# Optimization experiments

Hardware: AMD Instinct MI355X
Metric: run time of the kernel (lower is better)

Reference implementation:

```python
import jax, jax.numpy as jnp
import numpy as np

B, F, T = 2, 512, 512
D, N, H = 1024, 16, 64   # hidden, heads, head_dim
K = 32                   # time-bias MLP kernal_size
FILT = 4096              # FFN filter size
L = 4                    # num_decoder_blocks
EPS = 1e-6


def _glorot(key, shape, fan_in, fan_out):
    lim = np.sqrt(6.0 / (fan_in + fan_out)).astype(np.float32)
    return jax.random.uniform(key, shape, jnp.float32, -lim, lim)


def setup_inputs() -> dict:
    key = jax.random.key(0)
    ks = jax.random.split(key, 18)
    inp = {
        'decoder_inputs': jax.random.normal(ks[0], (B, F, D), jnp.float32),
        'encoder_outputs': jax.random.normal(ks[1], (B, T, D), jnp.float32),
        'decoder_times_dist': jax.random.uniform(ks[2], (B, F, F), jnp.float32),
        'decoder_encoder_times_dist': jax.random.uniform(ks[3], (B, F, T), jnp.float32),
        'dec_self_attn_bias': jnp.zeros((B, 1, 1, F), jnp.float32),
        'enc_dec_attn_bias': jnp.zeros((B, 1, 1, T), jnp.float32),
        # per-block stacked parameters (leading dim L)
        'Wq': _glorot(ks[4], (L, D, N, H), D, D),
        'Wk': _glorot(ks[5], (L, D, N, H), D, D),
        'Wv': _glorot(ks[6], (L, D, N, H), D, D),
        'Wo': _glorot(ks[7], (L, N, H, D), D, D),
        'Wth': _glorot(ks[8], (L, 1, K), 1, K),
        'bth': jnp.zeros((L, K), jnp.float32),
        'Wto': _glorot(ks[9], (L, K, 1), K, 1),
        'bto': jnp.zeros((L, 1), jnp.float32),
        'Wf1': _glorot(ks[10], (L, D, FILT), D, FILT),
        'bf1': jnp.zeros((L, FILT), jnp.float32),
        'Wf2': _glorot(ks[11], (L, FILT, D), FILT, D),
        'bf2': jnp.zeros((L, D), jnp.float32),
    }
    return inp


def _norm(x):
    # non-trainable LayerNormalization: (x - mean) / (std + eps)
    m = jnp.mean(x, axis=-1, keepdims=True)
    s = jnp.sqrt(jnp.mean((x - m) ** 2, axis=-1, keepdims=True))
    return (x - m) / (s + EPS)


def _attention(x, src, dist, bias, Wq, Wk, Wv, Wo, Wth, bth, Wto, bto):
    q = jnp.einsum('bfd,dnh->bfnh', x, Wq) * (H ** -0.5)
    k = jnp.einsum('btd,dnh->btnh', src, Wk)
    v = jnp.einsum('btd,dnh->btnh', src, Wv)
    # learned time bias: [B,F,T,1] -> relu MLP(K) -> 1 -> [B,F,T]
    hbias = jax.nn.relu(dist[..., None] @ Wth + bth)        # [B,F,T,K]
    qs_bias = (hbias @ Wto + bto)[..., 0]                   # [B,F,T]
    logits = jnp.einsum('btnh,bfnh->bnft', k, q)            # [B,N,F,T]
    logits = logits + bias + qs_bias[:, None]
    w = jax.nn.softmax(logits, axis=-1)
    out = jnp.einsum('bnft,btnh->bfnh', w, v)
    return jnp.einsum('bfnh,nhd->bfd', out, Wo)


def reference(decoder_inputs, encoder_outputs, decoder_times_dist,
              decoder_encoder_times_dist, dec_self_attn_bias, enc_dec_attn_bias,
              Wq, Wk, Wv, Wo, Wth, bth, Wto, bto, Wf1, bf1, Wf2, bf2):
    # decoder_times_dist / dec_self_attn_bias are accepted but unused (as in source call)
    x = decoder_inputs
    for i in range(L):
        # enc-dec attention with pre-norm + residual
        y = _attention(_norm(x), encoder_outputs, decoder_encoder_times_dist,
                       enc_dec_attn_bias, Wq[i], Wk[i], Wv[i], Wo[i],
                       Wth[i], bth[i], Wto[i], bto[i])
        x = x + y
        # FFN with pre-norm + residual
        y = jax.nn.relu(_norm(x) @ Wf1[i] + bf1[i]) @ Wf2[i] + bf2[i]
        x = x + y
    return _norm(x)
```

## Files before the change

### kernel.cpp

```cpp
#include <hip/hip_runtime.h>

typedef unsigned short u16;
typedef __attribute__((ext_vector_type(8))) unsigned short u16x8;
typedef __attribute__((ext_vector_type(4))) unsigned short u16x4;
typedef __attribute__((ext_vector_type(4))) float f32x4;

#define DEVI __device__ __forceinline__

DEVI u16 f2bf(float f){
  unsigned u = __float_as_uint(f);
  u += 0x7FFFu + ((u >> 16) & 1u);
  return (u16)(u >> 16);
}

DEVI void gload16(const void* g, void* l){
  __builtin_amdgcn_global_load_lds((const __attribute__((address_space(1))) void*)g,
                                   (__attribute__((address_space(3))) void*)l, 16, 0, 0);
}

DEVI float wave_sum(float v){
#pragma unroll
  for (int o = 32; o; o >>= 1) v += __shfl_xor(v, o, 64);
  return v;
}

#define MFMA16(a,b,c) __builtin_amdgcn_mfma_f32_16x16x32_bf16((a),(b),(c),0,0,0)

__global__ __launch_bounds__(256) void f32_to_bf16_k(const float* __restrict__ in,
                                                     u16* __restrict__ out, int n4){
  int i = blockIdx.x * 256 + threadIdx.x;
  if (i < n4){
    float4 v = ((const float4*)in)[i];
    u16x4 o = { f2bf(v.x), f2bf(v.y), f2bf(v.z), f2bf(v.w) };
    ((u16x4*)out)[i] = o;
  }
}

__global__ __launch_bounds__(256) void trans_f32_bf16_k(const float* __restrict__ in0,
                                                        u16* __restrict__ out0, int R, int C){
  __shared__ u16 tile[32][33];
  const float* in = in0 + (size_t)blockIdx.z * R * C;
  u16* out = out0 + (size_t)blockIdx.z * R * C;
  const int c0 = blockIdx.x * 32, r0 = blockIdx.y * 32;
  const int tx = threadIdx.x & 31, ty = threadIdx.x >> 5;
#pragma unroll
  for (int k = 0; k < 4; k++)
    tile[ty + k*8][tx] = f2bf(in[(size_t)(r0 + ty + k*8) * C + c0 + tx]);
  __syncthreads();
#pragma unroll
  for (int k = 0; k < 4; k++)
    out[(size_t)(c0 + ty + k*8) * R + r0 + tx] = tile[tx][ty + k*8];
}

__global__ __launch_bounds__(256) void vtrans_k(const u16* __restrict__ V0, u16* __restrict__ Vt0){
  __shared__ u16 tile[32][33];
  const int t0 = blockIdx.x * 32;
  const int h0 = blockIdx.y * 32;
  const int z = blockIdx.z, l = z >> 5, bn = z & 31;
  const int b = bn >> 4, n = bn & 15;
  const u16* V = V0 + (size_t)l * 1048576;
  u16* Vt = Vt0 + (size_t)l * 1048576;
  const int tx = threadIdx.x & 31, ty = threadIdx.x >> 5;
#pragma unroll
  for (int k = 0; k < 4; k++)
    tile[ty + k*8][tx] = V[(size_t)(b*512 + t0 + ty + k*8) * 1024 + n*64 + h0 + tx];
  __syncthreads();
#pragma unroll
  for (int k = 0; k < 4; k++)
    Vt[(size_t)((b*16 + n)*64 + h0 + ty + k*8) * 512 + t0 + tx] = tile[tx][ty + k*8];
}

__global__ __launch_bounds__(256) void layernorm_k(const float* __restrict__ in, u16* __restrict__ outp){
  const int row = blockIdx.x;
  const int tid = threadIdx.x;
  const float4 v = ((const float4*)(in + (size_t)row * 1024))[tid];
  __shared__ float sb[8];
  const int wid = tid >> 6, lane = tid & 63;
  float s = wave_sum(v.x + v.y + v.z + v.w);
  if (lane == 0) sb[wid] = s;
  __syncthreads();
  const float mean = (sb[0] + sb[1] + sb[2] + sb[3]) * (1.0f / 1024.0f);
  const float dx = v.x - mean, dy = v.y - mean, dz = v.z - mean, dw = v.w - mean;
  float q = wave_sum(dx*dx + dy*dy + dz*dz + dw*dw);
  if (lane == 0) sb[4 + wid] = q;
  __syncthreads();
  const float sd = sqrtf((sb[4] + sb[5] + sb[6] + sb[7]) * (1.0f / 1024.0f));
  const float inv = 1.0f / (sd + 1e-6f);
  u16x4 o = { f2bf(dx*inv), f2bf(dy*inv), f2bf(dz*inv), f2bf(dw*inv) };
  ((u16x4*)outp)[(size_t)row * 256 + tid] = o;
}

__global__ __launch_bounds__(256) void qsbias_k(const float* __restrict__ dist,
    const float* __restrict__ Wth0, const float* __restrict__ bth0,
    const float* __restrict__ Wto0, const float* __restrict__ bto0,
    float* __restrict__ qs0){
  const int ly = blockIdx.y;
  const float* Wth = Wth0 + ly*32;
  const float* bth = bth0 + ly*32;
  const float* Wto = Wto0 + ly*32;
  float* qs = qs0 + (size_t)ly * 524288;
  const int idx = blockIdx.x * 256 + threadIdx.x;
  float4 s4 = ((const float4*)dist)[idx];
  float sv[4] = { s4.x, s4.y, s4.z, s4.w };
  float r[4];
  const float b0 = bto0[ly];
#pragma unroll
  for (int c = 0; c < 4; c++) r[c] = b0;
#pragma unroll
  for (int k = 0; k < 32; k++){
    const float wk = Wth[k], bk = bth[k], ok = Wto[k];
#pragma unroll
    for (int c = 0; c < 4; c++){
      float h = fmaxf(sv[c] * wk + bk, 0.0f);
      r[c] += h * ok;
    }
  }
  ((float4*)qs)[idx] = make_float4(r[0], r[1], r[2], r[3]);
}

template<int MODE>
DEVI void gemm128_core(const u16* A, int lda, const u16* Bt, int ldb,
                       int Klen, int Nd, void* Cout,
                       const float* bias, float scale,
                       u16* Als, u16* Bls, int row0, int col0){
  const int tid = threadIdx.x;
  const int wid = tid >> 6, lane = tid & 63;
  const int wm = wid >> 1, wn = wid & 1;
  const int lrow = lane & 15, g = lane >> 4, e7 = lane & 7;
  f32x4 acc[4][4] = {};

  const int scol = ((lane & 7) ^ ((lane >> 3) & 7)) * 8;
  const u16* Ag = A + (size_t)(row0 + wid*8 + (lane >> 3)) * lda + scol;
  const u16* Bg = Bt + (size_t)(col0 + wid*8 + (lane >> 3)) * ldb + scol;
  const int dst0 = wid * 512;

  const int nt = Klen >> 6;

#define STAGE128(buf, k0)                                                     \
  {                                                                           \
    _Pragma("unroll")                                                         \
    for (int q = 0; q < 4; q++){                                              \
      gload16(Ag + (size_t)q*32*lda + (k0), Als + (buf)*8192 + dst0 + q*2048);\
      gload16(Bg + (size_t)q*32*ldb + (k0), Bls + (buf)*8192 + dst0 + q*2048);\
    }                                                                         \
  }

  STAGE128(0, 0);
  __syncthreads();

  for (int t = 0; t < nt; t++){
    const int cur = t & 1;
    if (t + 1 < nt) STAGE128(cur ^ 1, (t + 1) << 6);
    const u16* Ab = Als + cur * 8192;
    const u16* Bb = Bls + cur * 8192;
#pragma unroll
    for (int ks = 0; ks < 2; ks++){
      const int sl = (((ks << 2) + g) ^ e7) << 3;
      u16x8 av[4], bv[4];
#pragma unroll
      for (int mi = 0; mi < 4; mi++)
        av[mi] = *(const u16x8*)(Ab + (wm*64 + mi*16 + lrow) * 64 + sl);
#pragma unroll
      for (int ni = 0; ni < 4; ni++)
        bv[ni] = *(const u16x8*)(Bb + (wn*64 + ni*16 + lrow) * 64 + sl);
#pragma unroll
      for (int mi = 0; mi < 4; mi++)
#pragma unroll
        for (int ni = 0; ni < 4; ni++)
          acc[mi][ni] = MFMA16(av[mi], bv[ni], acc[mi][ni]);
    }
    __syncthreads();
  }
#undef STAGE128

#pragma unroll
  for (int mi = 0; mi < 4; mi++){
#pragma unroll
    for (int ni = 0; ni < 4; ni++){
      const int col = col0 + wn*64 + ni*16 + lrow;
#pragma unroll
      for (int j = 0; j < 4; j++){
        const int row = row0 + wm*64 + mi*16 + g*4 + j;
        float v = acc[mi][ni][j];
        if (MODE == 3) v = fmaxf(v + bias[col], 0.0f);
        if (MODE == 0 || MODE == 3)
          ((u16*)Cout)[(size_t)row * Nd + col] = f2bf(v);
        else
          ((float*)Cout)[(size_t)row * Nd + col] = v;
      }
    }
  }
}

template<int MODE>
__global__ __launch_bounds__(256) void gemm128_k(const u16* __restrict__ A, int lda,
    const u16* __restrict__ Bt, int ldb, int Klen, int Nd, void* __restrict__ Cout,
    const float* __restrict__ bias, float scale){
  __shared__ __align__(16) u16 Als[2 * 8192];
  __shared__ __align__(16) u16 Bls[2 * 8192];
  gemm128_core<MODE>(A, lda, Bt, ldb, Klen, Nd, Cout, bias, scale,
                     Als, Bls, blockIdx.y * 128, blockIdx.x * 128);
}

__global__ __launch_bounds__(256) void gemmKV_k(const u16* __restrict__ encb,
    const u16* __restrict__ Wkt, const u16* __restrict__ Wvt,
    u16* __restrict__ Kb, u16* __restrict__ Vb){
  __shared__ __align__(16) u16 Als[2 * 8192];
  __shared__ __align__(16) u16 Bls[2 * 8192];
  const int z = blockIdx.z, l = z >> 1;
  const u16* Bt = ((z & 1) ? Wvt : Wkt) + (size_t)l * 1048576;
  u16* out = ((z & 1) ? Vb : Kb) + (size_t)l * 1048576;
  gemm128_core<0>(encb, 1024, Bt, 1024, 1024, 1024, out, nullptr, 1.0f,
                  Als, Bls, blockIdx.y * 128, blockIdx.x * 128);
}

__global__ __launch_bounds__(256) void gemm_splitk_k(const u16* __restrict__ A, int lda,
    const u16* __restrict__ Bt, int ldb, int Klen, float* __restrict__ part){
  __shared__ __align__(16) u16 Als[2 * 8192];
  __shared__ __align__(16) u16 Bls[2 * 8192];
  const int z = blockIdx.z;
  gemm128_core<5>(A + (size_t)z * Klen, lda, Bt + (size_t)z * Klen, ldb, Klen, 1024,
                  part + (size_t)z * 1048576, nullptr, 1.0f,
                  Als, Bls, blockIdx.y * 128, blockIdx.x * 128);
}

__global__ __launch_bounds__(256) void reduce4_bf16_k(const float* __restrict__ part,
                                                      u16* __restrict__ out, float scale){
  const int idx = blockIdx.x * 256 + threadIdx.x;
  float4 p0 = ((const float4*)part)[idx];
  float4 p1 = ((const float4*)(part + 1048576))[idx];
  float4 p2 = ((const float4*)(part + 2097152))[idx];
  float4 p3 = ((const float4*)(part + 3145728))[idx];
  u16x4 o = { f2bf((p0.x + p1.x + p2.x + p3.x) * scale),
              f2bf((p0.y + p1.y + p2.y + p3.y) * scale),
              f2bf((p0.z + p1.z + p2.z + p3.z) * scale),
              f2bf((p0.w + p1.w + p2.w + p3.w) * scale) };
  ((u16x4*)out)[idx] = o;
}

template<int BIAS, int LAST>
__global__ __launch_bounds__(256) void reduce_ln_k(const float* __restrict__ part,
    const float* __restrict__ bias, float* __restrict__ x, u16* __restrict__ xn,
    float* __restrict__ dout){
  const int row = blockIdx.x, tid = threadIdx.x;
  const size_t idx = (size_t)row * 256 + tid;
  float4 v = ((const float4*)x)[idx];
  float4 p0 = ((const float4*)part)[idx];
  float4 p1 = ((const float4*)(part + 1048576))[idx];
  float4 p2 = ((const float4*)(part + 2097152))[idx];
  float4 p3 = ((const float4*)(part + 3145728))[idx];
  v.x += p0.x + p1.x + p2.x + p3.x;
  v.y += p0.y + p1.y + p2.y + p3.y;
  v.z += p0.z + p1.z + p2.z + p3.z;
  v.w += p0.w + p1.w + p2.w + p3.w;
  if (BIAS){
    const float4 b = *(const float4*)(bias + tid * 4);
    v.x += b.x; v.y += b.y; v.z += b.z; v.w += b.w;
  }
  if (!LAST) ((float4*)x)[idx] = v;

  __shared__ float sb[8];
  const int wid = tid >> 6, lane = tid & 63;
  float s = wave_sum(v.x + v.y + v.z + v.w);
  if (lane == 0) sb[wid] = s;
  __syncthreads();
  const float mean = (sb[0] + sb[1] + sb[2] + sb[3]) * (1.0f / 1024.0f);
  const float dx = v.x - mean, dy = v.y - mean, dz = v.z - mean, dw = v.w - mean;
  float q = wave_sum(dx*dx + dy*dy + dz*dz + dw*dw);
  if (lane == 0) sb[4 + wid] = q;
  __syncthreads();
  const float sd = sqrtf((sb[4] + sb[5] + sb[6] + sb[7]) * (1.0f / 1024.0f));
  const float inv = 1.0f / (sd + 1e-6f);
  if (LAST){
    ((float4*)dout)[idx] = make_float4(dx*inv, dy*inv, dz*inv, dw*inv);
  } else {
    u16x4 o = { f2bf(dx*inv), f2bf(dy*inv), f2bf(dz*inv), f2bf(dw*inv) };
    ((u16x4*)xn)[idx] = o;
  }
}

__global__ __launch_bounds__(256, 1) void attn_k(const u16* __restrict__ Q,
    const u16* __restrict__ Kb, const u16* __restrict__ Vt,
    const float* __restrict__ qs, const float* __restrict__ abias,
    u16* __restrict__ aout){
  const int n = blockIdx.x, f0 = blockIdx.y * 64, b = blockIdx.z;
  const int w = threadIdx.x >> 6, lane = threadIdx.x & 63;
  const int l15 = lane & 15, g = lane >> 4, e7 = lane & 7;
  const int fw = f0 + w * 16;
  __shared__ __align__(16) u16 Pl[4][16 * 512];
  u16* pw = &Pl[w][0];

  const u16* qp = Q + ((size_t)b*512 + fw + l15) * 1024 + n*64 + g*8;
  const u16x8 qf0 = *(const u16x8*)qp;
  const u16x8 qf1 = *(const u16x8*)(qp + 32);

  f32x4 acc[32];
  const u16* kp = Kb + ((size_t)b*512 + l15) * 1024 + n*64 + g*8;
#pragma unroll
  for (int tf = 0; tf < 32; tf++){
    u16x8 k0 = *(const u16x8*)(kp + (size_t)tf*16*1024);
    u16x8 k1 = *(const u16x8*)(kp + (size_t)tf*16*1024 + 32);
    f32x4 z = {0.f, 0.f, 0.f, 0.f};
    z = MFMA16(k0, qf0, z);
    acc[tf] = MFMA16(k1, qf1, z);
  }

  const float* qsp = qs + ((size_t)b*512 + fw + l15) * 512 + g*4;
  const float* abp = abias + (size_t)b*512 + g*4;
  float m = -3.0e38f;
#pragma unroll
  for (int tf = 0; tf < 32; tf++){
    float4 qv = *(const float4*)(qsp + tf*16);
    float4 av = *(const float4*)(abp + tf*16);
    acc[tf][0] += qv.x + av.x;
    acc[tf][1] += qv.y + av.y;
    acc[tf][2] += qv.z + av.z;
    acc[tf][3] += qv.w + av.w;
    m = fmaxf(m, fmaxf(fmaxf(acc[tf][0], acc[tf][1]), fmaxf(acc[tf][2], acc[tf][3])));
  }
  m = fmaxf(m, __shfl_xor(m, 16, 64));
  m = fmaxf(m, __shfl_xor(m, 32, 64));

  float s = 0.f;
#pragma unroll
  for (int tf = 0; tf < 32; tf++){
#pragma unroll
    for (int j = 0; j < 4; j++){
      float e = __expf(acc[tf][j] - m);
      acc[tf][j] = e; s += e;
    }
  }
  s += __shfl_xor(s, 16, 64);
  s += __shfl_xor(s, 32, 64);
  const float inv = 1.0f / s;
  float invj[4];
#pragma unroll
  for (int j = 0; j < 4; j++) invj[j] = __shfl(inv, g*4 + j, 64);

#pragma unroll
  for (int tf = 0; tf < 32; tf++){
    const int chunk = tf*2 + (g >> 1);
    const int boff = (l15 << 10) + ((chunk ^ e7) << 4) + ((g & 1) << 3);
    u16x4 pk = { f2bf(acc[tf][0]), f2bf(acc[tf][1]), f2bf(acc[tf][2]), f2bf(acc[tf][3]) };
    *(u16x4*)((char*)pw + boff) = pk;
  }

  f32x4 oacc[4] = {};
  const u16* vp = Vt + ((size_t)(b*16 + n)*64 + l15) * 512 + g*8;
  for (int kk = 0; kk < 16; kk++){
    u16x8 pa = *(const u16x8*)((char*)pw + (l15 << 10) + ((((kk << 2) + g) ^ e7) << 4));
#pragma unroll
    for (int nf = 0; nf < 4; nf++){
      u16x8 vb = *(const u16x8*)(vp + (size_t)nf*16*512 + kk*32);
      oacc[nf] = MFMA16(pa, vb, oacc[nf]);
    }
  }

  u16* op = aout + ((size_t)b*512 + fw + g*4) * 1024 + n*64 + l15;
#pragma unroll
  for (int nf = 0; nf < 4; nf++)
#pragma unroll
    for (int j = 0; j < 4; j++)
      op[(size_t)j*1024 + nf*16] = f2bf(oacc[nf][j] * invj[j]);
}

extern "C" void kernel_launch(void* const* d_in, const int* in_sizes, int n_in,
                              void* d_out, int out_size, void* d_ws, size_t ws_size,
                              hipStream_t stream){
  const float* dec_in   = (const float*)d_in[0];
  const float* enc      = (const float*)d_in[1];
  const float* dist     = (const float*)d_in[3];
  const float* abias    = (const float*)d_in[5];
  const float* Wq  = (const float*)d_in[6];
  const float* Wk  = (const float*)d_in[7];
  const float* Wv  = (const float*)d_in[8];
  const float* Wo  = (const float*)d_in[9];
  const float* Wth = (const float*)d_in[10];
  const float* bth = (const float*)d_in[11];
  const float* Wto = (const float*)d_in[12];
  const float* bto = (const float*)d_in[13];
  const float* Wf1 = (const float*)d_in[14];
  const float* bf1 = (const float*)d_in[15];
  const float* Wf2 = (const float*)d_in[16];
  const float* bf2 = (const float*)d_in[17];
  float* dout = (float*)d_out;

  char* wp = (char*)d_ws;
  auto alloc = [&](size_t n) -> char* {
    char* p = wp; wp += (n + 255) & ~(size_t)255; return p;
  };
  float* x     = (float*)alloc((size_t)1048576 * 4);
  u16*  xn     = (u16*)alloc((size_t)1048576 * 2);
  u16*  encb   = (u16*)alloc((size_t)1048576 * 2);
  u16*  Wqt    = (u16*)alloc((size_t)4194304 * 2);
  u16*  Wkt    = (u16*)alloc((size_t)4194304 * 2);
  u16*  Wvt    = (u16*)alloc((size_t)4194304 * 2);
  u16*  Wot    = (u16*)alloc((size_t)4194304 * 2);
  u16*  Wf1t   = (u16*)alloc((size_t)16777216 * 2);
  u16*  Wf2t   = (u16*)alloc((size_t)16777216 * 2);
  u16*  Kb     = (u16*)alloc((size_t)4194304 * 2);
  u16*  Vb     = (u16*)alloc((size_t)4194304 * 2);
  u16*  Vt     = (u16*)alloc((size_t)4194304 * 2);
  u16*  Qb     = (u16*)alloc((size_t)1048576 * 2);
  float* qs    = (float*)alloc((size_t)2097152 * 4);
  u16*  aout   = (u16*)alloc((size_t)1048576 * 2);
  u16*  ffh    = (u16*)alloc((size_t)4194304 * 2);
  float* part  = (float*)alloc((size_t)4194304 * 4);

  hipMemcpyAsync(x, dec_in, (size_t)1048576 * 4, hipMemcpyDeviceToDevice, stream);
  f32_to_bf16_k<<<1024, 256, 0, stream>>>(enc, encb, 262144);

  trans_f32_bf16_k<<<dim3(32, 32, 4), 256, 0, stream>>>(Wq, Wqt, 1024, 1024);
  trans_f32_bf16_k<<<dim3(32, 32, 4), 256, 0, stream>>>(Wk, Wkt, 1024, 1024);
  trans_f32_bf16_k<<<dim3(32, 32, 4), 256, 0, stream>>>(Wv, Wvt, 1024, 1024);
  trans_f32_bf16_k<<<dim3(32, 32, 4), 256, 0, stream>>>(Wo, Wot, 1024, 1024);
  trans_f32_bf16_k<<<dim3(128, 32, 4), 256, 0, stream>>>(Wf1, Wf1t, 1024, 4096);
  trans_f32_bf16_k<<<dim3(32, 128, 4), 256, 0, stream>>>(Wf2, Wf2t, 4096, 1024);

  qsbias_k<<<dim3(512, 4), 256, 0, stream>>>(dist, Wth, bth, Wto, bto, qs);

  gemmKV_k<<<dim3(8, 8, 8), 256, 0, stream>>>(encb, Wkt, Wvt, Kb, Vb);
  vtrans_k<<<dim3(16, 2, 128), 256, 0, stream>>>(Vb, Vt);

  layernorm_k<<<1024, 256, 0, stream>>>(x, xn);

  for (int i = 0; i < 4; i++){
    const size_t wo = (size_t)i * 1048576;

    gemm_splitk_k<<<dim3(8, 8, 4), 256, 0, stream>>>(xn, 1024, Wqt + wo, 1024, 256, part);
    reduce4_bf16_k<<<1024, 256, 0, stream>>>(part, Qb, 0.125f);

    attn_k<<<dim3(16, 8, 2), 256, 0, stream>>>(Qb, Kb + wo, Vt + wo,
                                               qs + (size_t)i * 524288, abias, aout);

    gemm_splitk_k<<<dim3(8, 8, 4), 256, 0, stream>>>(aout, 1024, Wot + wo, 1024, 256, part);
    reduce_ln_k<0, 0><<<1024, 256, 0, stream>>>(part, nullptr, x, xn, nullptr);

    gemm128_k<3><<<dim3(32, 8), 256, 0, stream>>>(xn, 1024, Wf1t + (size_t)i*4194304, 1024,
                                                  1024, 4096, ffh, bf1 + (size_t)i*4096, 1.0f);
    gemm_splitk_k<<<dim3(8, 8, 4), 256, 0, stream>>>(ffh, 4096, Wf2t + (size_t)i*4194304, 4096,
                                                     1024, part);
    if (i < 3)
      reduce_ln_k<1, 0><<<1024, 256, 0, stream>>>(part, bf2 + (size_t)i*1024, x, xn, nullptr);
    else
      reduce_ln_k<1, 1><<<1024, 256, 0, stream>>>(part, bf2 + (size_t)i*1024, x, nullptr, dout);
  }
}
```

Measured before the change: 535.9 us.

## Shrink GEMM N-tile to 64, fold Q split-K reduce into attention, batch weight transposes

All GEMMs now use a 128x64 tile instead of 128x128, which doubles the grid size and gives more blocks to fill the device's CUs on these small problems. The separate reduce kernel for the Q projection is removed, and attention sums the four fp32 split-K partials and applies the scale directly when it loads Q. The four attention-weight transposes become one launch. In exchange, each GEMM block reuses its loaded data less, and every attention block reads fp32 partials from global memory redundantly.

```diff
diff --git a/kernel.cpp b/kernel.cpp
--- a/kernel.cpp
+++ b/kernel.cpp
@@ -50,6 +50,26 @@
 #pragma unroll
   for (int k = 0; k < 4; k++)
     out[(size_t)(c0 + ty + k*8) * R + r0 + tx] = tile[tx][ty + k*8];
+}
+
+__global__ __launch_bounds__(256) void trans4_f32_bf16_k(
+    const float* __restrict__ Wq, const float* __restrict__ Wk,
+    const float* __restrict__ Wv, const float* __restrict__ Wo,
+    u16* __restrict__ Wqt, u16* __restrict__ Wkt,
+    u16* __restrict__ Wvt, u16* __restrict__ Wot){
+  __shared__ u16 tile[32][33];
+  const int z = blockIdx.z, sel = z >> 2, l = z & 3;
+  const float* in = (sel == 0 ? Wq : sel == 1 ? Wk : sel == 2 ? Wv : Wo) + (size_t)l * 1048576;
+  u16* out = (sel == 0 ? Wqt : sel == 1 ? Wkt : sel == 2 ? Wvt : Wot) + (size_t)l * 1048576;
+  const int c0 = blockIdx.x * 32, r0 = blockIdx.y * 32;
+  const int tx = threadIdx.x & 31, ty = threadIdx.x >> 5;
+#pragma unroll
+  for (int k = 0; k < 4; k++)
+    tile[ty + k*8][tx] = f2bf(in[(size_t)(r0 + ty + k*8) * 1024 + c0 + tx]);
+  __syncthreads();
+#pragma unroll
+  for (int k = 0; k < 4; k++)
+    out[(size_t)(c0 + ty + k*8) * 1024 + r0 + tx] = tile[tx][ty + k*8];
 }
 
 __global__ __launch_bounds__(256) void vtrans_k(const u16* __restrict__ V0, u16* __restrict__ Vt0){
@@ -118,16 +138,18 @@
   ((float4*)qs)[idx] = make_float4(r[0], r[1], r[2], r[3]);
 }
 
-template<int MODE>
+template<int MODE, int BN>
 DEVI void gemm128_core(const u16* A, int lda, const u16* Bt, int ldb,
                        int Klen, int Nd, void* Cout,
                        const float* bias, float scale,
                        u16* Als, u16* Bls, int row0, int col0){
+  constexpr int WN = BN / 2, FN = BN / 32;
+  constexpr int BSZ = BN * 64;
   const int tid = threadIdx.x;
   const int wid = tid >> 6, lane = tid & 63;
   const int wm = wid >> 1, wn = wid & 1;
   const int lrow = lane & 15, g = lane >> 4, e7 = lane & 7;
-  f32x4 acc[4][4] = {};
+  f32x4 acc[4][FN] = {};
 
   const int scol = ((lane & 7) ^ ((lane >> 3) & 7)) * 8;
   const u16* Ag = A + (size_t)(row0 + wid*8 + (lane >> 3)) * lda + scol;
@@ -139,10 +161,11 @@
 #define STAGE128(buf, k0)                                                     \
   {                                                                           \
     _Pragma("unroll")                                                         \
-    for (int q = 0; q < 4; q++){                                              \
+    for (int q = 0; q < 4; q++)                                               \
       gload16(Ag + (size_t)q*32*lda + (k0), Als + (buf)*8192 + dst0 + q*2048);\
-      gload16(Bg + (size_t)q*32*ldb + (k0), Bls + (buf)*8192 + dst0 + q*2048);\
-    }                                                                         \
+    _Pragma("unroll")                                                         \
+    for (int q = 0; q < BN/32; q++)                                           \
+      gload16(Bg + (size_t)q*32*ldb + (k0), Bls + (buf)*BSZ + dst0 + q*2048); \
   }
 
   STAGE128(0, 0);
@@ -152,21 +175,21 @@
     const int cur = t & 1;
     if (t + 1 < nt) STAGE128(cur ^ 1, (t + 1) << 6);
     const u16* Ab = Als + cur * 8192;
-    const u16* Bb = Bls + cur * 8192;
+    const u16* Bb = Bls + cur * BSZ;
 #pragma unroll
     for (int ks = 0; ks < 2; ks++){
       const int sl = (((ks << 2) + g) ^ e7) << 3;
-      u16x8 av[4], bv[4];
+      u16x8 av[4], bv[FN];
 #pragma unroll
       for (int mi = 0; mi < 4; mi++)
         av[mi] = *(const u16x8*)(Ab + (wm*64 + mi*16 + lrow) * 64 + sl);
 #pragma unroll
-      for (int ni = 0; ni < 4; ni++)
-        bv[ni] = *(const u16x8*)(Bb + (wn*64 + ni*16 + lrow) * 64 + sl);
+      for (int ni = 0; ni < FN; ni++)
+        bv[ni] = *(const u16x8*)(Bb + (wn*WN + ni*16 + lrow) * 64 + sl);
 #pragma unroll
       for (int mi = 0; mi < 4; mi++)
 #pragma unroll
-        for (int ni = 0; ni < 4; ni++)
+        for (int ni = 0; ni < FN; ni++)
           acc[mi][ni] = MFMA16(av[mi], bv[ni], acc[mi][ni]);
     }
     __syncthreads();
@@ -176,8 +199,8 @@
 #pragma unroll
   for (int mi = 0; mi < 4; mi++){
 #pragma unroll
-    for (int ni = 0; ni < 4; ni++){
-      const int col = col0 + wn*64 + ni*16 + lrow;
+    for (int ni = 0; ni < FN; ni++){
+      const int col = col0 + wn*WN + ni*16 + lrow;
 #pragma unroll
       for (int j = 0; j < 4; j++){
         const int row = row0 + wm*64 + mi*16 + g*4 + j;
@@ -197,45 +220,31 @@
     const u16* __restrict__ Bt, int ldb, int Klen, int Nd, void* __restrict__ Cout,
     const float* __restrict__ bias, float scale){
   __shared__ __align__(16) u16 Als[2 * 8192];
-  __shared__ __align__(16) u16 Bls[2 * 8192];
-  gemm128_core<MODE>(A, lda, Bt, ldb, Klen, Nd, Cout, bias, scale,
-                     Als, Bls, blockIdx.y * 128, blockIdx.x * 128);
+  __shared__ __align__(16) u16 Bls[2 * 4096];
+  gemm128_core<MODE, 64>(A, lda, Bt, ldb, Klen, Nd, Cout, bias, scale,
+                         Als, Bls, blockIdx.y * 128, blockIdx.x * 64);
 }
 
 __global__ __launch_bounds__(256) void gemmKV_k(const u16* __restrict__ encb,
     const u16* __restrict__ Wkt, const u16* __restrict__ Wvt,
     u16* __restrict__ Kb, u16* __restrict__ Vb){
   __shared__ __align__(16) u16 Als[2 * 8192];
-  __shared__ __align__(16) u16 Bls[2 * 8192];
+  __shared__ __align__(16) u16 Bls[2 * 4096];
   const int z = blockIdx.z, l = z >> 1;
   const u16* Bt = ((z & 1) ? Wvt : Wkt) + (size_t)l * 1048576;
   u16* out = ((z & 1) ? Vb : Kb) + (size_t)l * 1048576;
-  gemm128_core<0>(encb, 1024, Bt, 1024, 1024, 1024, out, nullptr, 1.0f,
-                  Als, Bls, blockIdx.y * 128, blockIdx.x * 128);
+  gemm128_core<0, 64>(encb, 1024, Bt, 1024, 1024, 1024, out, nullptr, 1.0f,
+                      Als, Bls, blockIdx.y * 128, blockIdx.x * 64);
 }
 
 __global__ __launch_bounds__(256) void gemm_splitk_k(const u16* __restrict__ A, int lda,
     const u16* __restrict__ Bt, int ldb, int Klen, float* __restrict__ part){
   __shared__ __align__(16) u16 Als[2 * 8192];
-  __shared__ __align__(16) u16 Bls[2 * 8192];
+  __shared__ __align__(16) u16 Bls[2 * 4096];
   const int z = blockIdx.z;
-  gemm128_core<5>(A + (size_t)z * Klen, lda, Bt + (size_t)z * Klen, ldb, Klen, 1024,
-                  part + (size_t)z * 1048576, nullptr, 1.0f,
-                  Als, Bls, blockIdx.y * 128, blockIdx.x * 128);
-}
-
-__global__ __launch_bounds__(256) void reduce4_bf16_k(const float* __restrict__ part,
-                                                      u16* __restrict__ out, float scale){
-  const int idx = blockIdx.x * 256 + threadIdx.x;
-  float4 p0 = ((const float4*)part)[idx];
-  float4 p1 = ((const float4*)(part + 1048576))[idx];
-  float4 p2 = ((const float4*)(part + 2097152))[idx];
-  float4 p3 = ((const float4*)(part + 3145728))[idx];
-  u16x4 o = { f2bf((p0.x + p1.x + p2.x + p3.x) * scale),
-              f2bf((p0.y + p1.y + p2.y + p3.y) * scale),
-              f2bf((p0.z + p1.z + p2.z + p3.z) * scale),
-              f2bf((p0.w + p1.w + p2.w + p3.w) * scale) };
-  ((u16x4*)out)[idx] = o;
+  gemm128_core<5, 64>(A + (size_t)z * Klen, lda, Bt + (size_t)z * Klen, ldb, Klen, 1024,
+                      part + (size_t)z * 1048576, nullptr, 1.0f,
+                      Als, Bls, blockIdx.y * 128, blockIdx.x * 64);
 }
 
 template<int BIAS, int LAST>
@@ -279,7 +288,7 @@
   }
 }
 
-__global__ __launch_bounds__(256, 1) void attn_k(const u16* __restrict__ Q,
+__global__ __launch_bounds__(256, 1) void attn_k(const float* __restrict__ partQ,
     const u16* __restrict__ Kb, const u16* __restrict__ Vt,
     const float* __restrict__ qs, const float* __restrict__ abias,
     u16* __restrict__ aout){
@@ -290,9 +299,22 @@
   __shared__ __align__(16) u16 Pl[4][16 * 512];
   u16* pw = &Pl[w][0];
 
-  const u16* qp = Q + ((size_t)b*512 + fw + l15) * 1024 + n*64 + g*8;
-  const u16x8 qf0 = *(const u16x8*)qp;
-  const u16x8 qf1 = *(const u16x8*)(qp + 32);
+  u16x8 qf0, qf1;
+  {
+    const float* pq = partQ + ((size_t)b*512 + fw + l15) * 1024 + n*64 + g*8;
+    float q0[8] = {0,0,0,0,0,0,0,0}, q1[8] = {0,0,0,0,0,0,0,0};
+#pragma unroll
+    for (int z = 0; z < 4; z++){
+      const float* p = pq + (size_t)z * 1048576;
+#pragma unroll
+      for (int e = 0; e < 8; e++){ q0[e] += p[e]; q1[e] += p[e + 32]; }
+    }
+#pragma unroll
+    for (int e = 0; e < 8; e++){
+      qf0[e] = f2bf(q0[e] * 0.125f);
+      qf1[e] = f2bf(q1[e] * 0.125f);
+    }
+  }
 
   f32x4 acc[32];
   const u16* kp = Kb + ((size_t)b*512 + l15) * 1024 + n*64 + g*8;
@@ -401,7 +423,6 @@
   u16*  Kb     = (u16*)alloc((size_t)4194304 * 2);
   u16*  Vb     = (u16*)alloc((size_t)4194304 * 2);
   u16*  Vt     = (u16*)alloc((size_t)4194304 * 2);
-  u16*  Qb     = (u16*)alloc((size_t)1048576 * 2);
   float* qs    = (float*)alloc((size_t)2097152 * 4);
   u16*  aout   = (u16*)alloc((size_t)1048576 * 2);
   u16*  ffh    = (u16*)alloc((size_t)4194304 * 2);
@@ -410,16 +431,13 @@
   hipMemcpyAsync(x, dec_in, (size_t)1048576 * 4, hipMemcpyDeviceToDevice, stream);
   f32_to_bf16_k<<<1024, 256, 0, stream>>>(enc, encb, 262144);
 
-  trans_f32_bf16_k<<<dim3(32, 32, 4), 256, 0, stream>>>(Wq, Wqt, 1024, 1024);
-  trans_f32_bf16_k<<<dim3(32, 32, 4), 256, 0, stream>>>(Wk, Wkt, 1024, 1024);
-  trans_f32_bf16_k<<<dim3(32, 32, 4), 256, 0, stream>>>(Wv, Wvt, 1024, 1024);
-  trans_f32_bf16_k<<<dim3(32, 32, 4), 256, 0, stream>>>(Wo, Wot, 1024, 1024);
+  trans4_f32_bf16_k<<<dim3(32, 32, 16), 256, 0, stream>>>(Wq, Wk, Wv, Wo, Wqt, Wkt, Wvt, Wot);
   trans_f32_bf16_k<<<dim3(128, 32, 4), 256, 0, stream>>>(Wf1, Wf1t, 1024, 4096);
   trans_f32_bf16_k<<<dim3(32, 128, 4), 256, 0, stream>>>(Wf2, Wf2t, 4096, 1024);
 
   qsbias_k<<<dim3(512, 4), 256, 0, stream>>>(dist, Wth, bth, Wto, bto, qs);
 
-  gemmKV_k<<<dim3(8, 8, 8), 256, 0, stream>>>(encb, Wkt, Wvt, Kb, Vb);
+  gemmKV_k<<<dim3(16, 8, 8), 256, 0, stream>>>(encb, Wkt, Wvt, Kb, Vb);
   vtrans_k<<<dim3(16, 2, 128), 256, 0, stream>>>(Vb, Vt);
 
   layernorm_k<<<1024, 256, 0, stream>>>(x, xn);
@@ -427,19 +445,18 @@
   for (int i = 0; i < 4; i++){
     const size_t wo = (size_t)i * 1048576;
 
-    gemm_splitk_k<<<dim3(8, 8, 4), 256, 0, stream>>>(xn, 1024, Wqt + wo, 1024, 256, part);
-    reduce4_bf16_k<<<1024, 256, 0, stream>>>(part, Qb, 0.125f);
-
-    attn_k<<<dim3(16, 8, 2), 256, 0, stream>>>(Qb, Kb + wo, Vt + wo,
+    gemm_splitk_k<<<dim3(16, 8, 4), 256, 0, stream>>>(xn, 1024, Wqt + wo, 1024, 256, part);
+
+    attn_k<<<dim3(16, 8, 2), 256, 0, stream>>>(part, Kb + wo, Vt + wo,
                                                qs + (size_t)i * 524288, abias, aout);
 
-    gemm_splitk_k<<<dim3(8, 8, 4), 256, 0, stream>>>(aout, 1024, Wot + wo, 1024, 256, part);
+    gemm_splitk_k<<<dim3(16, 8, 4), 256, 0, stream>>>(aout, 1024, Wot + wo, 1024, 256, part);
     reduce_ln_k<0, 0><<<1024, 256, 0, stream>>>(part, nullptr, x, xn, nullptr);
 
-    gemm128_k<3><<<dim3(32, 8), 256, 0, stream>>>(xn, 1024, Wf1t + (size_t)i*4194304, 1024,
+    gemm128_k<3><<<dim3(64, 8), 256, 0, stream>>>(xn, 1024, Wf1t + (size_t)i*4194304, 1024,
                                                   1024, 4096, ffh, bf1 + (size_t)i*4096, 1.0f);
-    gemm_splitk_k<<<dim3(8, 8, 4), 256, 0, stream>>>(ffh, 4096, Wf2t + (size_t)i*4194304, 4096,
-                                                     1024, part);
+    gemm_splitk_k<<<dim3(16, 8, 4), 256, 0, stream>>>(ffh, 4096, Wf2t + (size_t)i*4194304, 4096,
+                                                      1024, part);
     if (i < 3)
       reduce_ln_k<1, 0><<<1024, 256, 0, stream>>>(part, bf2 + (size_t)i*1024, x, xn, nullptr);
     else
```

New measurement: 489.1 us. 8.7% less time.
